# Kernel tuning notes

Hardware: AMD Instinct MI355X
Metric: run time of the kernel (lower is better)

Reference implementation:

```python
import jax, jax.numpy as jnp
import numpy as np

N = 100000
E = 1600000
IN_DIM, HID, OUT = 128, 64, 32
SLOPE = 0.1


def setup_inputs() -> dict:
    key = jax.random.key(0)
    ks = jax.random.split(key, 8)
    x = jax.random.normal(ks[0], (N, IN_DIM), dtype=jnp.float32)
    edge_index = jax.random.randint(ks[1], (2, E), 0, N, dtype=jnp.int64)
    s1 = 1.0 / np.sqrt(IN_DIM)
    s2 = 1.0 / np.sqrt(HID)
    W_l1 = jax.random.uniform(ks[2], (IN_DIM, HID), jnp.float32, -s1, s1)
    W_r1 = jax.random.uniform(ks[3], (IN_DIM, HID), jnp.float32, -s1, s1)
    b1 = jax.random.uniform(ks[4], (HID,), jnp.float32, -s1, s1)
    W_l2 = jax.random.uniform(ks[5], (HID, OUT), jnp.float32, -s2, s2)
    W_r2 = jax.random.uniform(ks[6], (HID, OUT), jnp.float32, -s2, s2)
    b2 = jax.random.uniform(ks[7], (OUT,), jnp.float32, -s2, s2)
    return {"x": x, "edge_index": edge_index,
            "W_l1": W_l1, "W_r1": W_r1, "b1": b1,
            "W_l2": W_l2, "W_r2": W_r2, "b2": b2}


def _sage_conv(h, src, dst, deg_inv, W_l, W_r, b):
    # mean-aggregate neighbor features: gather from src, scatter-add to dst
    agg = jax.ops.segment_sum(h[src], dst, num_segments=N) * deg_inv  # [N, d]
    return agg @ W_l + h @ W_r + b


def reference(x, edge_index, W_l1, W_r1, b1, W_l2, W_r2, b2):
    src, dst = edge_index[0], edge_index[1]
    deg = jax.ops.segment_sum(jnp.ones((E,), x.dtype), dst, num_segments=N)
    deg_inv = (1.0 / jnp.maximum(deg, 1.0))[:, None]  # [N, 1]
    h = jax.nn.leaky_relu(_sage_conv(x, src, dst, deg_inv, W_l1, W_r1, b1), SLOPE)
    z = jax.nn.leaky_relu(_sage_conv(h, src, dst, deg_inv, W_l2, W_r2, b2), SLOPE)
    return z
```

## Files before the change

kernel.cpp:

```cpp
#include <hip/hip_runtime.h>


constexpr int IN_DIM  = 128;
constexpr int HID     = 64;
constexpr int OUT_DIM = 32;
constexpr float SLOPE = 0.1f;
constexpr int NPB_SHIFT = 8;
constexpr int NBMAX = 512;
constexpr int CHUNK = 4096;
constexpr int HIST_BLOCKS = 256;
constexpr int SUBCAP = 4096;

typedef unsigned int uint32;
typedef unsigned short ushort16;

__device__ inline float blo(uint32 u) { return __uint_as_float(u << 16); }
__device__ inline float bhi(uint32 u) { return __uint_as_float(u & 0xffff0000u); }
__device__ inline ushort16 f2b(float f) {
    uint32 u = __float_as_uint(f);
    u += 0x7fffu + ((u >> 16) & 1u);
    return (ushort16)(u >> 16);
}
__device__ inline uint32 pack2(float lo, float hi) {
    return (uint32)f2b(lo) | ((uint32)f2b(hi) << 16);
}
__device__ inline float lrelu(float v) { return (v > 0.f) ? v : SLOPE * v; }
__device__ inline void addup(float* acc, uint4 u) {
    acc[0] += blo(u.x); acc[1] += bhi(u.x);
    acc[2] += blo(u.y); acc[3] += bhi(u.y);
    acc[4] += blo(u.z); acc[5] += bhi(u.z);
    acc[6] += blo(u.w); acc[7] += bhi(u.w);
}

__global__ __launch_bounds__(256) void prep_kernel(
    const float* __restrict__ Wl1, const float* __restrict__ Wr1,
    const float* __restrict__ Wl2, const float* __restrict__ Wr2,
    ushort16* __restrict__ Wb1, ushort16* __restrict__ Wb2,
    int* __restrict__ bhist) {
    const int gid = blockIdx.x * 256 + threadIdx.x;
    if (gid < NBMAX) bhist[gid] = 0;
    for (int i = gid; i < 128 * 128; i += gridDim.x * 256) {
        int c = i >> 7, k = i & 127;
        Wb1[i] = f2b((c < HID) ? Wl1[k * HID + c] : Wr1[k * HID + (c - HID)]);
    }
    for (int i = gid; i < 64 * 64; i += gridDim.x * 256) {
        int c = i >> 6, k = i & 63;
        Wb2[i] = f2b((c < OUT_DIM) ? Wl2[k * OUT_DIM + c]
                                   : Wr2[k * OUT_DIM + (c - OUT_DIM)]);
    }
}

__global__ __launch_bounds__(256) void gemm1_hist_kernel(
    const float* __restrict__ x, const ushort16* __restrict__ Wb1,
    const float* __restrict__ b1,
    const int* __restrict__ dst, int* __restrict__ bhist,
    ushort16* __restrict__ xl, float* __restrict__ xr,
    int N, int E, int ngemm) {
    using frag = __attribute__((ext_vector_type(8))) short;
    using f32x4 = __attribute__((ext_vector_type(4))) float;
    constexpr int LDA = IN_DIM + 8;
    __shared__ ushort16 Ash[64][LDA];
    const int tid = threadIdx.x;
    if (blockIdx.x >= ngemm) {
        int* bh = (int*)Ash;
        for (int i = tid; i < NBMAX; i += 256) bh[i] = 0;
        __syncthreads();
        const int b0 = blockIdx.x - ngemm;
        for (int e = b0 * 256 + tid; e < E; e += HIST_BLOCKS * 256)
            atomicAdd(&bh[dst[e] >> NPB_SHIFT], 1);
        __syncthreads();
        for (int b = tid; b < NBMAX; b += 256)
            if (bh[b]) atomicAdd(&bhist[b], bh[b]);
        return;
    }
    const int n0 = blockIdx.x * 64;
    {
        const int lc = (tid & 31) * 4;
        for (int row = tid >> 5; row < 64; row += 8) {
            int node = n0 + row;
            float4 xv = (node < N)
                ? *reinterpret_cast<const float4*>(&x[(long)node * IN_DIM + lc])
                : float4{0.f, 0.f, 0.f, 0.f};
            ushort16 pk[4] = {f2b(xv.x), f2b(xv.y), f2b(xv.z), f2b(xv.w)};
            *reinterpret_cast<ushort2*>(&Ash[row][lc])     = ushort2{pk[0], pk[1]};
            *reinterpret_cast<ushort2*>(&Ash[row][lc + 2]) = ushort2{pk[2], pk[3]};
        }
    }
    __syncthreads();
    const int lane = tid & 63;
    const int m0   = (tid >> 6) * 16;
    const int mlo  = lane & 15;
    const int qk   = lane >> 4;
    frag Af[4];
#pragma unroll
    for (int kc = 0; kc < 4; ++kc)
        Af[kc] = *reinterpret_cast<const frag*>(&Ash[m0 + mlo][kc * 32 + qk * 8]);
#pragma unroll
    for (int ct = 0; ct < 8; ++ct) {
        f32x4 acc = {0.f, 0.f, 0.f, 0.f};
#pragma unroll
        for (int kc = 0; kc < 4; ++kc) {
            frag Bf = *reinterpret_cast<const frag*>(
                &Wb1[(ct * 16 + mlo) * 128 + kc * 32 + qk * 8]);
            acc = __builtin_amdgcn_mfma_f32_16x16x32_bf16(Af[kc], Bf, acc, 0, 0, 0);
        }
        const int col = ct * 16 + mlo;
#pragma unroll
        for (int r = 0; r < 4; ++r) {
            int node = n0 + m0 + qk * 4 + r;
            if (node < N) {
                if (col < HID) xl[(long)node * HID + col] = f2b(acc[r]);
                else           xr[(long)node * HID + (col - HID)] = acc[r] + b1[col - HID];
            }
        }
    }
}

__global__ __launch_bounds__(512) void bucket_scan_kernel(
    const int* __restrict__ bhist, int* __restrict__ pbase,
    int* __restrict__ bcur, int NB) {
    __shared__ int s2[512];
    const int t = threadIdx.x;
    int bh = (t < NB) ? bhist[t] : 0;
    int pd = (bh + 15) & ~15;
    s2[t] = pd; __syncthreads();
    for (int off = 1; off < 512; off <<= 1) {
        int b = (t >= off) ? s2[t - off] : 0;
        __syncthreads();
        s2[t] += b;
        __syncthreads();
    }
    pbase[t] = s2[t] - pd;
    bcur[t]  = s2[t] - pd;
}

__global__ __launch_bounds__(256) void partition_kernel(
    const int* __restrict__ src, const int* __restrict__ dst,
    int* __restrict__ bcur, uint32* __restrict__ pairs, int E, int NB) {
    __shared__ int hist[NBMAX], loff[NBMAX], cur[NBMAX], gbase[NBMAX];
    __shared__ int s[256];
    __shared__ uint32 stage[CHUNK];
    const int tid = threadIdx.x;
    const int e0  = blockIdx.x * CHUNK;
    const int cnt = min(CHUNK, E - e0);
    for (int i = tid; i < NBMAX; i += 256) hist[i] = 0;
    __syncthreads();
    int sreg[16], dreg[16];
#pragma unroll
    for (int k = 0; k < 16; ++k) {
        int i = tid + k * 256;
        if (i < cnt) {
            sreg[k] = src[e0 + i];
            dreg[k] = dst[e0 + i];
            atomicAdd(&hist[dreg[k] >> NPB_SHIFT], 1);
        }
    }
    __syncthreads();
    int a0 = hist[2 * tid], a1 = hist[2 * tid + 1];
    s[tid] = a0 + a1; __syncthreads();
    for (int off = 1; off < 256; off <<= 1) {
        int t = (tid >= off) ? s[tid - off] : 0;
        __syncthreads();
        s[tid] += t;
        __syncthreads();
    }
    int ex = s[tid] - (a0 + a1);
    loff[2 * tid] = ex;      loff[2 * tid + 1] = ex + a0;
    cur[2 * tid]  = ex;      cur[2 * tid + 1]  = ex + a0;
    __syncthreads();
#pragma unroll
    for (int k = 0; k < 16; ++k) {
        int i = tid + k * 256;
        if (i < cnt) {
            int b = dreg[k] >> NPB_SHIFT;
            int pos = atomicAdd(&cur[b], 1);
            stage[pos] = (uint32)sreg[k] | ((uint32)(dreg[k] & 255) << 24);
        }
    }
    __syncthreads();
    for (int b = tid; b < NB; b += 256) {
        int cb = hist[b];
        if (cb) gbase[b] = atomicAdd(&bcur[b], cb);
    }
    __syncthreads();
    for (int i = tid; i < cnt; i += 256) {
        int lo = 0, hi = NB - 1;
        while (lo < hi) {
            int mid = (lo + hi + 1) >> 1;
            if (loff[mid] <= i) lo = mid; else hi = mid - 1;
        }
        pairs[gbase[lo] + (i - loff[lo])] = stage[i];
    }
}

__global__ __launch_bounds__(512) void agg1_sort_kernel(
    const uint32* __restrict__ pairs, const int* __restrict__ bhist,
    const int* __restrict__ pbase,
    const uint4* __restrict__ xlq, const float* __restrict__ xr,
    uint32* __restrict__ srcs, int* __restrict__ rowptr, int* __restrict__ degA,
    uint4* __restrict__ hq, int N) {
    __shared__ int hist[256], loff[256], cur[128];
    __shared__ int lsrc[SUBCAP];
    const int tid  = threadIdx.x;
    const int bkt  = blockIdx.x >> 1;
    const int half = blockIdx.x & 1;
    const int n0   = bkt << NPB_SHIFT;
    const int base = pbase[bkt];
    const int sz   = bhist[bkt];
    if (tid < 256) hist[tid] = 0;
    __syncthreads();
    for (int i = tid; i < sz; i += 512)
        atomicAdd(&hist[pairs[base + i] >> 24], 1);
    __syncthreads();
    int v = (tid < 256) ? hist[tid] : 0;
    if (tid < 256) loff[tid] = v;
    __syncthreads();
    for (int off = 1; off < 256; off <<= 1) {
        int t = (tid >= off && tid < 256) ? loff[tid - off] : 0;
        __syncthreads();
        if (tid < 256) loff[tid] += t;
        __syncthreads();
    }
    if (tid < 256) loff[tid] -= v;
    __syncthreads();
    if (half == 0 && tid < 256 && n0 + tid < N) {
        rowptr[n0 + tid] = base + loff[tid];
        degA[n0 + tid]   = hist[tid];
    }
    const int hbase = loff[half << 7];
    const int hcnt  = (half ? sz : loff[128]) - hbase;
    if (tid < 128) cur[tid] = loff[(half << 7) + tid] - hbase;
    __syncthreads();
    for (int i = tid; i < sz; i += 512) {
        uint32 u = pairs[base + i];
        int dl = u >> 24;
        if ((dl >> 7) == half) {
            int pos = atomicAdd(&cur[dl & 127], 1);
            lsrc[pos] = (int)(u & 0xFFFFFFu);
        }
    }
    __syncthreads();
    for (int i = tid; i < hcnt; i += 512)
        srcs[base + hbase + i] = (uint32)lsrc[i];
    const int lane = tid & 63;
    const int wid  = tid >> 6;
    const int li   = lane & 7;
#pragma unroll
    for (int pass = 0; pass < 2; ++pass) {
        const int nl = (half << 7) + pass * 64 + wid * 8 + (lane >> 3);
        const int n  = n0 + nl;
        if (n >= N) continue;
        const int lo0 = loff[nl] - hbase;
        const int d   = hist[nl];
        float acc[8] = {};
        int j = 0;
        while (j + 16 <= d) {
            int i0[8], i1[8];
#pragma unroll
            for (int t = 0; t < 8; ++t) i0[t] = lsrc[lo0 + j + t];
#pragma unroll
            for (int t = 0; t < 8; ++t) i1[t] = lsrc[lo0 + j + 8 + t];
            uint4 u0[8], u1[8];
#pragma unroll
            for (int t = 0; t < 8; ++t) u0[t] = xlq[(long)i0[t] * 8 + li];
#pragma unroll
            for (int t = 0; t < 8; ++t) u1[t] = xlq[(long)i1[t] * 8 + li];
#pragma unroll
            for (int t = 0; t < 8; ++t) { addup(acc, u0[t]); addup(acc, u1[t]); }
            j += 16;
        }
        if (j + 8 <= d) {
            int i0[8];
#pragma unroll
            for (int t = 0; t < 8; ++t) i0[t] = lsrc[lo0 + j + t];
            uint4 u0[8];
#pragma unroll
            for (int t = 0; t < 8; ++t) u0[t] = xlq[(long)i0[t] * 8 + li];
#pragma unroll
            for (int t = 0; t < 8; ++t) addup(acc, u0[t]);
            j += 8;
        }
        for (; j < d; ++j) {
            uint4 u = xlq[(long)lsrc[lo0 + j] * 8 + li];
            addup(acc, u);
        }
        const float dinv = (d > 0) ? (1.f / (float)d) : 1.f;
        float4 xrA = *reinterpret_cast<const float4*>(&xr[(long)n * HID + 8 * li]);
        float4 xrB = *reinterpret_cast<const float4*>(&xr[(long)n * HID + 8 * li + 4]);
        float h[8];
        h[0] = fmaf(acc[0], dinv, xrA.x); h[1] = fmaf(acc[1], dinv, xrA.y);
        h[2] = fmaf(acc[2], dinv, xrA.z); h[3] = fmaf(acc[3], dinv, xrA.w);
        h[4] = fmaf(acc[4], dinv, xrB.x); h[5] = fmaf(acc[5], dinv, xrB.y);
        h[6] = fmaf(acc[6], dinv, xrB.z); h[7] = fmaf(acc[7], dinv, xrB.w);
#pragma unroll
        for (int t = 0; t < 8; ++t) h[t] = lrelu(h[t]);
        uint4 pk;
        pk.x = pack2(h[0], h[1]); pk.y = pack2(h[2], h[3]);
        pk.z = pack2(h[4], h[5]); pk.w = pack2(h[6], h[7]);
        hq[(long)n * 8 + li] = pk;
    }
}

__global__ __launch_bounds__(256) void gemm2_mfma_kernel(
    const ushort16* __restrict__ hs, const ushort16* __restrict__ Wb2,
    const float* __restrict__ b2,
    ushort16* __restrict__ hl, float* __restrict__ hr, int N) {
    using frag = __attribute__((ext_vector_type(8))) short;
    using f32x4 = __attribute__((ext_vector_type(4))) float;
    const int tid  = threadIdx.x;
    const int n0   = blockIdx.x * 64;
    const int lane = tid & 63;
    const int m0   = (tid >> 6) * 16;
    const int mlo  = lane & 15;
    const int qk   = lane >> 4;
    const int row  = n0 + m0 + mlo;
    const int arow = (row < N) ? row : 0;
    frag Af[2];
#pragma unroll
    for (int kc = 0; kc < 2; ++kc)
        Af[kc] = *reinterpret_cast<const frag*>(&hs[(long)arow * HID + kc * 32 + qk * 8]);
#pragma unroll
    for (int ct = 0; ct < 4; ++ct) {
        f32x4 acc = {0.f, 0.f, 0.f, 0.f};
#pragma unroll
        for (int kc = 0; kc < 2; ++kc) {
            frag Bf = *reinterpret_cast<const frag*>(
                &Wb2[(ct * 16 + mlo) * 64 + kc * 32 + qk * 8]);
            acc = __builtin_amdgcn_mfma_f32_16x16x32_bf16(Af[kc], Bf, acc, 0, 0, 0);
        }
        const int col = ct * 16 + mlo;
#pragma unroll
        for (int r = 0; r < 4; ++r) {
            int node = n0 + m0 + qk * 4 + r;
            if (node < N) {
                if (col < OUT_DIM) hl[(long)node * OUT_DIM + col] = f2b(acc[r]);
                else hr[(long)node * OUT_DIM + (col - OUT_DIM)] = acc[r] + b2[col - OUT_DIM];
            }
        }
    }
}

__global__ __launch_bounds__(256) void agg2_final_kernel(
    const int* __restrict__ rowptr, const int* __restrict__ degA,
    const uint32* __restrict__ srcs,
    const uint4* __restrict__ hlq, const float* __restrict__ hr,
    float* __restrict__ z, int N) {
    const int lane  = threadIdx.x & 63;
    const int li    = lane & 3;
    const int gbase = lane & 60;
    const int wave  = (blockIdx.x << 2) + (threadIdx.x >> 6);
    const int n     = wave * 16 + (lane >> 2);
    if (n >= N) return;
    const int rp = rowptr[n];
    const int d  = degA[n];
    float acc[8] = {};
    int j = 0;
    while (j + 16 <= d) {
        int sA = (int)srcs[rp + j + li];
        int sB = (int)srcs[rp + j + 4 + li];
        int sC = (int)srcs[rp + j + 8 + li];
        int sD = (int)srcs[rp + j + 12 + li];
        uint4 u[16];
#pragma unroll
        for (int t = 0; t < 4; ++t) u[t]      = hlq[(long)__shfl(sA, gbase + t) * 4 + li];
#pragma unroll
        for (int t = 0; t < 4; ++t) u[4 + t]  = hlq[(long)__shfl(sB, gbase + t) * 4 + li];
#pragma unroll
        for (int t = 0; t < 4; ++t) u[8 + t]  = hlq[(long)__shfl(sC, gbase + t) * 4 + li];
#pragma unroll
        for (int t = 0; t < 4; ++t) u[12 + t] = hlq[(long)__shfl(sD, gbase + t) * 4 + li];
#pragma unroll
        for (int t = 0; t < 16; ++t) addup(acc, u[t]);
        j += 16;
    }
    while (j + 4 <= d) {
        int sA = (int)srcs[rp + j + li];
        uint4 u[4];
#pragma unroll
        for (int t = 0; t < 4; ++t) u[t] = hlq[(long)__shfl(sA, gbase + t) * 4 + li];
#pragma unroll
        for (int t = 0; t < 4; ++t) addup(acc, u[t]);
        j += 4;
    }
    int r = d - j;
    if (r > 0) {
        int sA = (int)srcs[rp + j + ((li < r) ? li : 0)];
#pragma unroll
        for (int t = 0; t < 3; ++t) {
            if (t < r) {
                uint4 u = hlq[(long)__shfl(sA, gbase + t) * 4 + li];
                addup(acc, u);
            }
        }
    }
    const float dinv = (d > 0) ? (1.f / (float)d) : 1.f;
    float4 hA = *reinterpret_cast<const float4*>(&hr[(long)n * OUT_DIM + 8 * li]);
    float4 hB = *reinterpret_cast<const float4*>(&hr[(long)n * OUT_DIM + 8 * li + 4]);
    float4 vA, vB;
    vA.x = lrelu(fmaf(acc[0], dinv, hA.x)); vA.y = lrelu(fmaf(acc[1], dinv, hA.y));
    vA.z = lrelu(fmaf(acc[2], dinv, hA.z)); vA.w = lrelu(fmaf(acc[3], dinv, hA.w));
    vB.x = lrelu(fmaf(acc[4], dinv, hB.x)); vB.y = lrelu(fmaf(acc[5], dinv, hB.y));
    vB.z = lrelu(fmaf(acc[6], dinv, hB.z)); vB.w = lrelu(fmaf(acc[7], dinv, hB.w));
    *reinterpret_cast<float4*>(&z[(long)n * OUT_DIM + 8 * li]) = vA;
    *reinterpret_cast<float4*>(&z[(long)n * OUT_DIM + 8 * li + 4]) = vB;
}

extern "C" void kernel_launch(void* const* d_in, const int* in_sizes, int n_in,
                              void* d_out, int out_size, void* d_ws, size_t ws_size,
                              hipStream_t stream) {
    const float* x   = (const float*)d_in[0];
    const int*   ei  = (const int*)d_in[1];
    const float* Wl1 = (const float*)d_in[2];
    const float* Wr1 = (const float*)d_in[3];
    const float* b1  = (const float*)d_in[4];
    const float* Wl2 = (const float*)d_in[5];
    const float* Wr2 = (const float*)d_in[6];
    const float* b2  = (const float*)d_in[7];

    const int N = in_sizes[0] / IN_DIM;
    const int E = in_sizes[1] / 2;
    const int* src = ei;
    const int* dst = ei + E;
    const int NB = (N + 255) >> NPB_SHIFT;

    char* p = (char*)d_ws;
    int* bhist    = (int*)p;           p += sizeof(int) * NBMAX;
    int* pbase    = (int*)p;           p += sizeof(int) * NBMAX;
    int* bcur     = (int*)p;           p += sizeof(int) * NBMAX;
    int* rowptr   = (int*)p;           p += sizeof(int) * (N + 4);
    int* degA     = (int*)p;           p += sizeof(int) * (N + 4);
    uint32* pairs = (uint32*)p;        p += sizeof(uint32) * ((size_t)E + 16 * NBMAX);
    uint32* srcs  = (uint32*)p;        p += sizeof(uint32) * ((size_t)E + 16 * NBMAX);
    ushort16* Wb1 = (ushort16*)p;      p += sizeof(ushort16) * 128 * 128;
    ushort16* Wb2 = (ushort16*)p;      p += sizeof(ushort16) * 64 * 64;
    ushort16* xl  = (ushort16*)p;      p += sizeof(ushort16) * (size_t)N * HID;
    float* xr     = (float*)p;         p += sizeof(float) * (size_t)N * HID;
    ushort16* h   = (ushort16*)p;      p += sizeof(ushort16) * (size_t)N * HID;
    ushort16* hl  = (ushort16*)p;      p += sizeof(ushort16) * (size_t)N * OUT_DIM;
    float* hr     = (float*)p;         p += sizeof(float) * (size_t)N * OUT_DIM;

    const int ngemm = (N + 63) / 64;
    prep_kernel<<<32, 256, 0, stream>>>(Wl1, Wr1, Wl2, Wr2, Wb1, Wb2, bhist);
    gemm1_hist_kernel<<<ngemm + HIST_BLOCKS, 256, 0, stream>>>(
        x, Wb1, b1, dst, bhist, xl, xr, N, E, ngemm);
    bucket_scan_kernel<<<1, 512, 0, stream>>>(bhist, pbase, bcur, NB);
    partition_kernel<<<(E + CHUNK - 1) / CHUNK, 256, 0, stream>>>(src, dst, bcur, pairs, E, NB);
    agg1_sort_kernel<<<NB * 2, 512, 0, stream>>>(pairs, bhist, pbase,
                                                 (const uint4*)xl, xr,
                                                 srcs, rowptr, degA, (uint4*)h, N);
    gemm2_mfma_kernel<<<(N + 63) / 64, 256, 0, stream>>>(h, Wb2, b2, hl, hr, N);
    agg2_final_kernel<<<(N + 63) / 64, 256, 0, stream>>>(rowptr, degA, srcs,
                                                         (const uint4*)hl, hr,
                                                         (float*)d_out, N);
}
```

Before: 275.3 us.

## Restructure pipeline: fuse scan into histogram, partition with gemm1, gemm2 into agg1

The standalone bucket scan is folded into the histogram kernel using a last-block-done counter. Edge partitioning now runs in the same launch as the first GEMM through a shared-memory union. The second GEMM is fused into the first aggregation kernel, which stages h in LDS instead of writing it to global memory, and the gather splits each node's edges across two lane groups combined by a shuffle. This removes two launches and a full h round-trip, at the cost of more LDS per block and a grid-wide atomic handoff.

```diff
diff --git a/kernel.cpp b/kernel.cpp
--- a/kernel.cpp
+++ b/kernel.cpp
@@ -8,7 +8,6 @@
 constexpr int NPB_SHIFT = 8;
 constexpr int NBMAX = 512;
 constexpr int CHUNK = 4096;
-constexpr int HIST_BLOCKS = 256;
 constexpr int SUBCAP = 4096;
 
 typedef unsigned int uint32;
@@ -36,9 +35,10 @@
     const float* __restrict__ Wl1, const float* __restrict__ Wr1,
     const float* __restrict__ Wl2, const float* __restrict__ Wr2,
     ushort16* __restrict__ Wb1, ushort16* __restrict__ Wb2,
-    int* __restrict__ bhist) {
+    int* __restrict__ bhist, int* __restrict__ done) {
     const int gid = blockIdx.x * 256 + threadIdx.x;
     if (gid < NBMAX) bhist[gid] = 0;
+    if (gid == NBMAX) *done = 0;
     for (int i = gid; i < 128 * 128; i += gridDim.x * 256) {
         int c = i >> 7, k = i & 127;
         Wb1[i] = f2b((c < HID) ? Wl1[k * HID + c] : Wr1[k * HID + (c - HID)]);
@@ -50,30 +50,114 @@
     }
 }
 
-__global__ __launch_bounds__(256) void gemm1_hist_kernel(
+__global__ __launch_bounds__(256) void hist_scan_kernel(
+    const int* __restrict__ dst, int* __restrict__ bhist,
+    int* __restrict__ pbase, int* __restrict__ bcur,
+    int* __restrict__ done, int E, int NB) {
+    __shared__ int bh[NBMAX];
+    __shared__ int s2[256];
+    __shared__ int flag;
+    const int tid = threadIdx.x;
+    for (int i = tid; i < NBMAX; i += 256) bh[i] = 0;
+    __syncthreads();
+    for (int e = blockIdx.x * 256 + tid; e < E; e += gridDim.x * 256)
+        atomicAdd(&bh[dst[e] >> NPB_SHIFT], 1);
+    __syncthreads();
+    for (int b = tid; b < NBMAX; b += 256)
+        if (bh[b]) atomicAdd(&bhist[b], bh[b]);
+    __threadfence();
+    if (tid == 0) flag = (atomicAdd(done, 1) == (int)gridDim.x - 1) ? 1 : 0;
+    __syncthreads();
+    if (!flag) return;
+    __threadfence();
+    int v0 = atomicAdd(&bhist[2 * tid], 0);
+    int v1 = atomicAdd(&bhist[2 * tid + 1], 0);
+    int p0 = (v0 + 15) & ~15, p1 = (v1 + 15) & ~15;
+    s2[tid] = p0 + p1; __syncthreads();
+    for (int off = 1; off < 256; off <<= 1) {
+        int b = (tid >= off) ? s2[tid - off] : 0;
+        __syncthreads();
+        s2[tid] += b;
+        __syncthreads();
+    }
+    int base = s2[tid] - (p0 + p1);
+    pbase[2 * tid]     = base;      bcur[2 * tid]     = base;
+    pbase[2 * tid + 1] = base + p0; bcur[2 * tid + 1] = base + p0;
+}
+
+__global__ __launch_bounds__(256) void gemm1_part_kernel(
     const float* __restrict__ x, const ushort16* __restrict__ Wb1,
     const float* __restrict__ b1,
-    const int* __restrict__ dst, int* __restrict__ bhist,
+    const int* __restrict__ src, const int* __restrict__ dst,
+    int* __restrict__ bcur, uint32* __restrict__ pairs,
     ushort16* __restrict__ xl, float* __restrict__ xr,
-    int N, int E, int ngemm) {
+    int N, int E, int NB, int npart) {
     using frag = __attribute__((ext_vector_type(8))) short;
     using f32x4 = __attribute__((ext_vector_type(4))) float;
     constexpr int LDA = IN_DIM + 8;
-    __shared__ ushort16 Ash[64][LDA];
+    __shared__ union {
+        struct {
+            int hist[NBMAX], loff[NBMAX], cur[NBMAX], gbase[NBMAX];
+            int s[256];
+            uint32 stage[CHUNK];
+        } p;
+        ushort16 Ash[64][LDA];
+    } sm;
     const int tid = threadIdx.x;
-    if (blockIdx.x >= ngemm) {
-        int* bh = (int*)Ash;
-        for (int i = tid; i < NBMAX; i += 256) bh[i] = 0;
-        __syncthreads();
-        const int b0 = blockIdx.x - ngemm;
-        for (int e = b0 * 256 + tid; e < E; e += HIST_BLOCKS * 256)
-            atomicAdd(&bh[dst[e] >> NPB_SHIFT], 1);
-        __syncthreads();
-        for (int b = tid; b < NBMAX; b += 256)
-            if (bh[b]) atomicAdd(&bhist[b], bh[b]);
+    if (blockIdx.x < npart) {
+        const int e0  = blockIdx.x * CHUNK;
+        const int cnt = min(CHUNK, E - e0);
+        for (int i = tid; i < NBMAX; i += 256) sm.p.hist[i] = 0;
+        __syncthreads();
+        int sreg[16], dreg[16];
+#pragma unroll
+        for (int k = 0; k < 16; ++k) {
+            int i = tid + k * 256;
+            if (i < cnt) {
+                sreg[k] = src[e0 + i];
+                dreg[k] = dst[e0 + i];
+                atomicAdd(&sm.p.hist[dreg[k] >> NPB_SHIFT], 1);
+            }
+        }
+        __syncthreads();
+        int a0 = sm.p.hist[2 * tid], a1 = sm.p.hist[2 * tid + 1];
+        sm.p.s[tid] = a0 + a1; __syncthreads();
+        for (int off = 1; off < 256; off <<= 1) {
+            int t = (tid >= off) ? sm.p.s[tid - off] : 0;
+            __syncthreads();
+            sm.p.s[tid] += t;
+            __syncthreads();
+        }
+        int ex = sm.p.s[tid] - (a0 + a1);
+        sm.p.loff[2 * tid] = ex;      sm.p.loff[2 * tid + 1] = ex + a0;
+        sm.p.cur[2 * tid]  = ex;      sm.p.cur[2 * tid + 1]  = ex + a0;
+        __syncthreads();
+#pragma unroll
+        for (int k = 0; k < 16; ++k) {
+            int i = tid + k * 256;
+            if (i < cnt) {
+                int b = dreg[k] >> NPB_SHIFT;
+                int pos = atomicAdd(&sm.p.cur[b], 1);
+                sm.p.stage[pos] = (uint32)sreg[k] | ((uint32)(dreg[k] & 255) << 24);
+            }
+        }
+        __syncthreads();
+        for (int b = tid; b < NB; b += 256) {
+            int cb = sm.p.hist[b];
+            if (cb) sm.p.gbase[b] = atomicAdd(&bcur[b], cb);
+        }
+        __syncthreads();
+        for (int i = tid; i < cnt; i += 256) {
+            int lo = 0, hi = NB - 1;
+            while (lo < hi) {
+                int mid = (lo + hi + 1) >> 1;
+                if (sm.p.loff[mid] <= i) lo = mid; else hi = mid - 1;
+            }
+            pairs[sm.p.gbase[lo] + (i - sm.p.loff[lo])] = sm.p.stage[i];
+        }
         return;
     }
-    const int n0 = blockIdx.x * 64;
+    const int n0 = (blockIdx.x - npart) * 64;
     {
         const int lc = (tid & 31) * 4;
         for (int row = tid >> 5; row < 64; row += 8) {
@@ -82,8 +166,8 @@
                 ? *reinterpret_cast<const float4*>(&x[(long)node * IN_DIM + lc])
                 : float4{0.f, 0.f, 0.f, 0.f};
             ushort16 pk[4] = {f2b(xv.x), f2b(xv.y), f2b(xv.z), f2b(xv.w)};
-            *reinterpret_cast<ushort2*>(&Ash[row][lc])     = ushort2{pk[0], pk[1]};
-            *reinterpret_cast<ushort2*>(&Ash[row][lc + 2]) = ushort2{pk[2], pk[3]};
+            *reinterpret_cast<ushort2*>(&sm.Ash[row][lc])     = ushort2{pk[0], pk[1]};
+            *reinterpret_cast<ushort2*>(&sm.Ash[row][lc + 2]) = ushort2{pk[2], pk[3]};
         }
     }
     __syncthreads();
@@ -94,7 +178,7 @@
     frag Af[4];
 #pragma unroll
     for (int kc = 0; kc < 4; ++kc)
-        Af[kc] = *reinterpret_cast<const frag*>(&Ash[m0 + mlo][kc * 32 + qk * 8]);
+        Af[kc] = *reinterpret_cast<const frag*>(&sm.Ash[m0 + mlo][kc * 32 + qk * 8]);
 #pragma unroll
     for (int ct = 0; ct < 8; ++ct) {
         f32x4 acc = {0.f, 0.f, 0.f, 0.f};
@@ -116,91 +200,19 @@
     }
 }
 
-__global__ __launch_bounds__(512) void bucket_scan_kernel(
-    const int* __restrict__ bhist, int* __restrict__ pbase,
-    int* __restrict__ bcur, int NB) {
-    __shared__ int s2[512];
-    const int t = threadIdx.x;
-    int bh = (t < NB) ? bhist[t] : 0;
-    int pd = (bh + 15) & ~15;
-    s2[t] = pd; __syncthreads();
-    for (int off = 1; off < 512; off <<= 1) {
-        int b = (t >= off) ? s2[t - off] : 0;
-        __syncthreads();
-        s2[t] += b;
-        __syncthreads();
-    }
-    pbase[t] = s2[t] - pd;
-    bcur[t]  = s2[t] - pd;
-}
-
-__global__ __launch_bounds__(256) void partition_kernel(
-    const int* __restrict__ src, const int* __restrict__ dst,
-    int* __restrict__ bcur, uint32* __restrict__ pairs, int E, int NB) {
-    __shared__ int hist[NBMAX], loff[NBMAX], cur[NBMAX], gbase[NBMAX];
-    __shared__ int s[256];
-    __shared__ uint32 stage[CHUNK];
-    const int tid = threadIdx.x;
-    const int e0  = blockIdx.x * CHUNK;
-    const int cnt = min(CHUNK, E - e0);
-    for (int i = tid; i < NBMAX; i += 256) hist[i] = 0;
-    __syncthreads();
-    int sreg[16], dreg[16];
-#pragma unroll
-    for (int k = 0; k < 16; ++k) {
-        int i = tid + k * 256;
-        if (i < cnt) {
-            sreg[k] = src[e0 + i];
-            dreg[k] = dst[e0 + i];
-            atomicAdd(&hist[dreg[k] >> NPB_SHIFT], 1);
-        }
-    }
-    __syncthreads();
-    int a0 = hist[2 * tid], a1 = hist[2 * tid + 1];
-    s[tid] = a0 + a1; __syncthreads();
-    for (int off = 1; off < 256; off <<= 1) {
-        int t = (tid >= off) ? s[tid - off] : 0;
-        __syncthreads();
-        s[tid] += t;
-        __syncthreads();
-    }
-    int ex = s[tid] - (a0 + a1);
-    loff[2 * tid] = ex;      loff[2 * tid + 1] = ex + a0;
-    cur[2 * tid]  = ex;      cur[2 * tid + 1]  = ex + a0;
-    __syncthreads();
-#pragma unroll
-    for (int k = 0; k < 16; ++k) {
-        int i = tid + k * 256;
-        if (i < cnt) {
-            int b = dreg[k] >> NPB_SHIFT;
-            int pos = atomicAdd(&cur[b], 1);
-            stage[pos] = (uint32)sreg[k] | ((uint32)(dreg[k] & 255) << 24);
-        }
-    }
-    __syncthreads();
-    for (int b = tid; b < NB; b += 256) {
-        int cb = hist[b];
-        if (cb) gbase[b] = atomicAdd(&bcur[b], cb);
-    }
-    __syncthreads();
-    for (int i = tid; i < cnt; i += 256) {
-        int lo = 0, hi = NB - 1;
-        while (lo < hi) {
-            int mid = (lo + hi + 1) >> 1;
-            if (loff[mid] <= i) lo = mid; else hi = mid - 1;
-        }
-        pairs[gbase[lo] + (i - loff[lo])] = stage[i];
-    }
-}
-
-__global__ __launch_bounds__(512) void agg1_sort_kernel(
+__global__ __launch_bounds__(512) void agg1_gemm2_kernel(
     const uint32* __restrict__ pairs, const int* __restrict__ bhist,
     const int* __restrict__ pbase,
     const uint4* __restrict__ xlq, const float* __restrict__ xr,
+    const ushort16* __restrict__ Wb2, const float* __restrict__ b2,
     uint32* __restrict__ srcs, int* __restrict__ rowptr, int* __restrict__ degA,
-    uint4* __restrict__ hq, int N) {
+    ushort16* __restrict__ hl, float* __restrict__ hr, int N) {
+    using frag = __attribute__((ext_vector_type(8))) short;
+    using f32x4 = __attribute__((ext_vector_type(4))) float;
+    constexpr int LDH = HID + 8;
     __shared__ int hist[256], loff[256], cur[128];
     __shared__ int lsrc[SUBCAP];
+    __shared__ ushort16 hsh[128][LDH];
     const int tid  = threadIdx.x;
     const int bkt  = blockIdx.x >> 1;
     const int half = blockIdx.x & 1;
@@ -245,80 +257,64 @@
     const int lane = tid & 63;
     const int wid  = tid >> 6;
     const int li   = lane & 7;
-#pragma unroll
-    for (int pass = 0; pass < 2; ++pass) {
-        const int nl = (half << 7) + pass * 64 + wid * 8 + (lane >> 3);
-        const int n  = n0 + nl;
-        if (n >= N) continue;
-        const int lo0 = loff[nl] - hbase;
-        const int d   = hist[nl];
-        float acc[8] = {};
-        int j = 0;
-        while (j + 16 <= d) {
-            int i0[8], i1[8];
-#pragma unroll
-            for (int t = 0; t < 8; ++t) i0[t] = lsrc[lo0 + j + t];
-#pragma unroll
-            for (int t = 0; t < 8; ++t) i1[t] = lsrc[lo0 + j + 8 + t];
-            uint4 u0[8], u1[8];
-#pragma unroll
-            for (int t = 0; t < 8; ++t) u0[t] = xlq[(long)i0[t] * 8 + li];
-#pragma unroll
-            for (int t = 0; t < 8; ++t) u1[t] = xlq[(long)i1[t] * 8 + li];
-#pragma unroll
-            for (int t = 0; t < 8; ++t) { addup(acc, u0[t]); addup(acc, u1[t]); }
-            j += 16;
-        }
-        if (j + 8 <= d) {
-            int i0[8];
-#pragma unroll
-            for (int t = 0; t < 8; ++t) i0[t] = lsrc[lo0 + j + t];
-            uint4 u0[8];
-#pragma unroll
-            for (int t = 0; t < 8; ++t) u0[t] = xlq[(long)i0[t] * 8 + li];
-#pragma unroll
-            for (int t = 0; t < 8; ++t) addup(acc, u0[t]);
-            j += 8;
-        }
-        for (; j < d; ++j) {
-            uint4 u = xlq[(long)lsrc[lo0 + j] * 8 + li];
-            addup(acc, u);
-        }
-        const float dinv = (d > 0) ? (1.f / (float)d) : 1.f;
-        float4 xrA = *reinterpret_cast<const float4*>(&xr[(long)n * HID + 8 * li]);
-        float4 xrB = *reinterpret_cast<const float4*>(&xr[(long)n * HID + 8 * li + 4]);
-        float h[8];
-        h[0] = fmaf(acc[0], dinv, xrA.x); h[1] = fmaf(acc[1], dinv, xrA.y);
-        h[2] = fmaf(acc[2], dinv, xrA.z); h[3] = fmaf(acc[3], dinv, xrA.w);
-        h[4] = fmaf(acc[4], dinv, xrB.x); h[5] = fmaf(acc[5], dinv, xrB.y);
-        h[6] = fmaf(acc[6], dinv, xrB.z); h[7] = fmaf(acc[7], dinv, xrB.w);
-#pragma unroll
-        for (int t = 0; t < 8; ++t) h[t] = lrelu(h[t]);
-        uint4 pk;
-        pk.x = pack2(h[0], h[1]); pk.y = pack2(h[2], h[3]);
-        pk.z = pack2(h[4], h[5]); pk.w = pack2(h[6], h[7]);
-        hq[(long)n * 8 + li] = pk;
-    }
-}
-
-__global__ __launch_bounds__(256) void gemm2_mfma_kernel(
-    const ushort16* __restrict__ hs, const ushort16* __restrict__ Wb2,
-    const float* __restrict__ b2,
-    ushort16* __restrict__ hl, float* __restrict__ hr, int N) {
-    using frag = __attribute__((ext_vector_type(8))) short;
-    using f32x4 = __attribute__((ext_vector_type(4))) float;
-    const int tid  = threadIdx.x;
-    const int n0   = blockIdx.x * 64;
-    const int lane = tid & 63;
-    const int m0   = (tid >> 6) * 16;
-    const int mlo  = lane & 15;
-    const int qk   = lane >> 4;
-    const int row  = n0 + m0 + mlo;
-    const int arow = (row < N) ? row : 0;
+    const int eh   = (lane >> 3) & 1;
+    const int nw   = lane >> 4;
+    for (int pass = 0; pass < 4; ++pass) {
+        const int nll = pass * 32 + wid * 4 + nw;
+        const int nl  = (half << 7) + nll;
+        const int n   = n0 + nl;
+        if (n < N) {
+            const int lo0 = loff[nl] - hbase;
+            const int d   = hist[nl];
+            const int jb  = eh ? (d >> 1) : 0;
+            const int je  = eh ? d : (d >> 1);
+            float acc[8] = {};
+            if (jb < je) {
+                int j = jb;
+                do {
+                    int i0[8];
+#pragma unroll
+                    for (int t = 0; t < 8; ++t) {
+                        int jj = j + t;
+                        i0[t] = lsrc[lo0 + (jj < je ? jj : je - 1)];
+                    }
+                    uint4 u0[8];
+#pragma unroll
+                    for (int t = 0; t < 8; ++t) u0[t] = xlq[(long)i0[t] * 8 + li];
+#pragma unroll
+                    for (int t = 0; t < 8; ++t)
+                        if (j + t < je) addup(acc, u0[t]);
+                    j += 8;
+                } while (j < je);
+            }
+#pragma unroll
+            for (int t = 0; t < 8; ++t) acc[t] += __shfl_xor(acc[t], 8);
+            if (eh == 0) {
+                const float dinv = (d > 0) ? (1.f / (float)d) : 1.f;
+                float4 xrA = *reinterpret_cast<const float4*>(&xr[(long)n * HID + 8 * li]);
+                float4 xrB = *reinterpret_cast<const float4*>(&xr[(long)n * HID + 8 * li + 4]);
+                float h[8];
+                h[0] = fmaf(acc[0], dinv, xrA.x); h[1] = fmaf(acc[1], dinv, xrA.y);
+                h[2] = fmaf(acc[2], dinv, xrA.z); h[3] = fmaf(acc[3], dinv, xrA.w);
+                h[4] = fmaf(acc[4], dinv, xrB.x); h[5] = fmaf(acc[5], dinv, xrB.y);
+                h[6] = fmaf(acc[6], dinv, xrB.z); h[7] = fmaf(acc[7], dinv, xrB.w);
+#pragma unroll
+                for (int t = 0; t < 8; ++t) h[t] = lrelu(h[t]);
+                uint4 pk;
+                pk.x = pack2(h[0], h[1]); pk.y = pack2(h[2], h[3]);
+                pk.z = pack2(h[4], h[5]); pk.w = pack2(h[6], h[7]);
+                *reinterpret_cast<uint4*>(&hsh[nll][li * 8]) = pk;
+            }
+        }
+    }
+    __syncthreads();
+    const int m0  = wid * 16;
+    const int mlo = lane & 15;
+    const int qk  = lane >> 4;
     frag Af[2];
 #pragma unroll
     for (int kc = 0; kc < 2; ++kc)
-        Af[kc] = *reinterpret_cast<const frag*>(&hs[(long)arow * HID + kc * 32 + qk * 8]);
+        Af[kc] = *reinterpret_cast<const frag*>(&hsh[m0 + mlo][kc * 32 + qk * 8]);
 #pragma unroll
     for (int ct = 0; ct < 4; ++ct) {
         f32x4 acc = {0.f, 0.f, 0.f, 0.f};
@@ -331,7 +327,7 @@
         const int col = ct * 16 + mlo;
 #pragma unroll
         for (int r = 0; r < 4; ++r) {
-            int node = n0 + m0 + qk * 4 + r;
+            int node = n0 + (half << 7) + m0 + qk * 4 + r;
             if (node < N) {
                 if (col < OUT_DIM) hl[(long)node * OUT_DIM + col] = f2b(acc[r]);
                 else hr[(long)node * OUT_DIM + (col - OUT_DIM)] = acc[r] + b2[col - OUT_DIM];
@@ -427,6 +423,7 @@
     int* bhist    = (int*)p;           p += sizeof(int) * NBMAX;
     int* pbase    = (int*)p;           p += sizeof(int) * NBMAX;
     int* bcur     = (int*)p;           p += sizeof(int) * NBMAX;
+    int* done     = (int*)p;           p += sizeof(int) * 4;
     int* rowptr   = (int*)p;           p += sizeof(int) * (N + 4);
     int* degA     = (int*)p;           p += sizeof(int) * (N + 4);
     uint32* pairs = (uint32*)p;        p += sizeof(uint32) * ((size_t)E + 16 * NBMAX);
@@ -435,20 +432,18 @@
     ushort16* Wb2 = (ushort16*)p;      p += sizeof(ushort16) * 64 * 64;
     ushort16* xl  = (ushort16*)p;      p += sizeof(ushort16) * (size_t)N * HID;
     float* xr     = (float*)p;         p += sizeof(float) * (size_t)N * HID;
-    ushort16* h   = (ushort16*)p;      p += sizeof(ushort16) * (size_t)N * HID;
     ushort16* hl  = (ushort16*)p;      p += sizeof(ushort16) * (size_t)N * OUT_DIM;
     float* hr     = (float*)p;         p += sizeof(float) * (size_t)N * OUT_DIM;
 
     const int ngemm = (N + 63) / 64;
-    prep_kernel<<<32, 256, 0, stream>>>(Wl1, Wr1, Wl2, Wr2, Wb1, Wb2, bhist);
-    gemm1_hist_kernel<<<ngemm + HIST_BLOCKS, 256, 0, stream>>>(
-        x, Wb1, b1, dst, bhist, xl, xr, N, E, ngemm);
-    bucket_scan_kernel<<<1, 512, 0, stream>>>(bhist, pbase, bcur, NB);
-    partition_kernel<<<(E + CHUNK - 1) / CHUNK, 256, 0, stream>>>(src, dst, bcur, pairs, E, NB);
-    agg1_sort_kernel<<<NB * 2, 512, 0, stream>>>(pairs, bhist, pbase,
-                                                 (const uint4*)xl, xr,
-                                                 srcs, rowptr, degA, (uint4*)h, N);
-    gemm2_mfma_kernel<<<(N + 63) / 64, 256, 0, stream>>>(h, Wb2, b2, hl, hr, N);
+    const int npart = (E + CHUNK - 1) / CHUNK;
+    prep_kernel<<<32, 256, 0, stream>>>(Wl1, Wr1, Wl2, Wr2, Wb1, Wb2, bhist, done);
+    hist_scan_kernel<<<256, 256, 0, stream>>>(dst, bhist, pbase, bcur, done, E, NB);
+    gemm1_part_kernel<<<npart + ngemm, 256, 0, stream>>>(
+        x, Wb1, b1, src, dst, bcur, pairs, xl, xr, N, E, NB, npart);
+    agg1_gemm2_kernel<<<NB * 2, 512, 0, stream>>>(pairs, bhist, pbase,
+                                                  (const uint4*)xl, xr, Wb2, b2,
+                                                  srcs, rowptr, degA, hl, hr, N);
     agg2_final_kernel<<<(N + 63) / 64, 256, 0, stream>>>(rowptr, degA, srcs,
                                                          (const uint4*)hl, hr,
                                                          (float*)d_out, N);
```

Result: no change. 275.0 us (-0.1%).
